# Kernel tuning notes

Hardware: AMD Instinct MI355X
Metric: run time of the kernel (lower is better)

The kernel has to match this reference:

```python
import jax, jax.numpy as jnp
import numpy as np

N_NODES = 50000
N_EDGES = 600000
F_IN = 128
F_OUT = 128


def setup_inputs() -> dict:
    key = jax.random.key(0)
    k1, k2, k3, k4 = jax.random.split(key, 4)
    x = jax.random.normal(k1, (N_NODES, F_IN), dtype=jnp.float32)
    edge_index = jax.random.randint(k2, (2, N_EDGES), 0, N_NODES, dtype=jnp.int64)
    # Linear weights stored as [in, out] so out = h @ W + b
    scale = 1.0 / np.sqrt(F_IN)
    W_l = jax.random.uniform(k3, (F_IN, F_OUT), jnp.float32, -scale, scale)
    W_r = jax.random.uniform(k4, (F_IN, F_OUT), jnp.float32, -scale, scale)
    b_l = jnp.zeros((F_OUT,), jnp.float32)
    b_r = jnp.zeros((F_OUT,), jnp.float32)
    return {"x": x, "edge_index": edge_index, "W_l": W_l, "b_l": b_l, "W_r": W_r, "b_r": b_r}


def reference(x, edge_index, W_l, b_l, W_r, b_r):
    num_nodes = x.shape[0]
    src, dst = edge_index[0], edge_index[1]
    # P2_Gather: source node features per edge  [E, F]
    x_j = x[src]
    # P3_ScatterAdd: sum over incoming edges per destination node  [N, F]
    sum_agg = jax.ops.segment_sum(x_j, dst, num_segments=num_nodes)
    # P3_ScatterAdd_Count: in-degree per node  [N]
    count = jax.ops.segment_sum(jnp.ones_like(dst, dtype=x.dtype), dst,
                                num_segments=num_nodes)
    # P4_ElewiseDiv: mean aggregation (avoid div-by-zero for isolated nodes)
    mean_agg = sum_agg / jnp.maximum(count, 1.0)[:, None]
    # P1_Matmul_Dual + P5_ElewiseAct
    out = mean_agg @ W_l + b_l + x @ W_r + b_r
    return jax.nn.relu(out)
```

## Files before the change

kernel.cpp:

```cpp
#include <hip/hip_runtime.h>

#define NN 50000
#define NE 600000
#define FD 128
#define MAXS 62

using short8  = __attribute__((ext_vector_type(8))) short;
using ushort8 = __attribute__((ext_vector_type(8))) unsigned short;
using f32x4   = __attribute__((ext_vector_type(4))) float;
using f32x2   = __attribute__((ext_vector_type(2))) float;

__device__ __forceinline__ unsigned short f2bf(float f) {
    unsigned int u = __float_as_uint(f);
    return (unsigned short)((u + 0x7FFFu + ((u >> 16) & 1u)) >> 16);
}
__device__ __forceinline__ float bf2f(unsigned short u) {
    return __uint_as_float(((unsigned int)u) << 16);
}

#if __has_builtin(__builtin_amdgcn_cvt_pk_f32_fp8) && __has_builtin(__builtin_amdgcn_cvt_pk_fp8_f32)
#define FP8_HW 1
#else
#define FP8_HW 0
#endif

__device__ __forceinline__ unsigned int sw_enc(float f) {
    unsigned u = __float_as_uint(f);
    unsigned s = (u >> 24) & 0x80u;
    unsigned a = u & 0x7FFFFFFFu;
    if (a < 0x3C800000u) return s;
    unsigned r = a + 0x7FFFFu + ((a >> 20) & 1u);
    unsigned e = r >> 23;
    unsigned m = (r >> 20) & 7u;
    return s | ((e - 120u) << 3) | m;
}
__device__ __forceinline__ float sw_dec(unsigned b) {
    unsigned em = b & 0x7Fu;
    unsigned u  = ((b & 0x80u) << 24) | ((em + 960u) << 20);
    return em ? __uint_as_float(u) : 0.0f;
}

__device__ __forceinline__ unsigned int enc4(float a, float b, float c, float d) {
#if FP8_HW
    unsigned int w = 0;
    w = __builtin_amdgcn_cvt_pk_fp8_f32(a, b, w, false);
    w = __builtin_amdgcn_cvt_pk_fp8_f32(c, d, w, true);
    return w;
#else
    return sw_enc(a) | (sw_enc(b) << 8) | (sw_enc(c) << 16) | (sw_enc(d) << 24);
#endif
}

__device__ __forceinline__ void dec4_fma(unsigned int dw, float w, float* a) {
#if FP8_HW
    f32x2 lo = __builtin_amdgcn_cvt_pk_f32_fp8(dw, false);
    f32x2 hi = __builtin_amdgcn_cvt_pk_f32_fp8(dw, true);
    a[0] = fmaf(w, lo[0], a[0]); a[1] = fmaf(w, lo[1], a[1]);
    a[2] = fmaf(w, hi[0], a[2]); a[3] = fmaf(w, hi[1], a[3]);
#else
    a[0] = fmaf(w, sw_dec(dw & 0xFFu),         a[0]);
    a[1] = fmaf(w, sw_dec((dw >> 8) & 0xFFu),  a[1]);
    a[2] = fmaf(w, sw_dec((dw >> 16) & 0xFFu), a[2]);
    a[3] = fmaf(w, sw_dec(dw >> 24),           a[3]);
#endif
}

#define OFF_SLOT  200192
#define OFF_XQ    6600192
#define OFF_XB    13000192
#define OFF_MEANB 25800192
#define OFF_WBT   38600192
#define WS_NEED   (38600192 + 65536)

#define NXB 3125
#define NWB 16
#define NZC 196

__global__ __launch_bounds__(256) void prep_k(const float* __restrict__ x,
                                              const float* __restrict__ Wl,
                                              const float* __restrict__ Wr,
                                              unsigned short* __restrict__ xb,
                                              unsigned int* __restrict__ xq,
                                              unsigned short* __restrict__ wbT,
                                              unsigned int* __restrict__ slotw) {
    int b = blockIdx.x;
    if (b < NXB) {
        int i = b * 256 + threadIdx.x;
        const float4* p = reinterpret_cast<const float4*>(x) + (size_t)i * 2;
        float4 a = p[0], c = p[1];
        short8 r;
        r[0] = (short)f2bf(a.x); r[1] = (short)f2bf(a.y);
        r[2] = (short)f2bf(a.z); r[3] = (short)f2bf(a.w);
        r[4] = (short)f2bf(c.x); r[5] = (short)f2bf(c.y);
        r[6] = (short)f2bf(c.z); r[7] = (short)f2bf(c.w);
        reinterpret_cast<short8*>(xb)[i] = r;
        uint2 q;
        q.x = enc4(a.x, a.y, a.z, a.w);
        q.y = enc4(c.x, c.y, c.z, c.w);
        reinterpret_cast<uint2*>(xq)[i] = q;
    } else if (b < NXB + NWB) {
        int u = (b - NXB) * 256 + threadIdx.x;
        int col = u & 127;
        int kb  = (u >> 7) * 8;
        short8 r;
        #pragma unroll
        for (int j = 0; j < 8; ++j) {
            int k = kb + j;
            float w = (k < 128) ? Wl[(size_t)k * FD + col]
                                : Wr[(size_t)(k - 128) * FD + col];
            r[j] = (short)f2bf(w);
        }
        *reinterpret_cast<short8*>(&wbT[col * 256 + kb]) = r;
    } else {
        int i = (b - NXB - NWB) * 256 + threadIdx.x;
        if (i < NN) slotw[(size_t)i * 32] = 0;
    }
}

__global__ __launch_bounds__(256) void scatter_slot_k(const int* __restrict__ ei,
                                                      unsigned int* __restrict__ slotw) {
    int e = blockIdx.x * 256 + threadIdx.x;
    if (e >= NE) return;
    int s = ei[e];
    int d = ei[NE + e];
    unsigned int* row = slotw + (size_t)d * 32;
    int p = atomicAdd((int*)row, 1);
    if (p < MAXS) reinterpret_cast<unsigned short*>(row)[2 + p] = (unsigned short)s;
}

__global__ __launch_bounds__(256) void gather_k(
    const unsigned int* __restrict__ xq,
    const unsigned int* __restrict__ slotw,
    unsigned short* __restrict__ meanb)
{
    int t = blockIdx.x * 256 + threadIdx.x;
    int n = t >> 3;
    if (n >= NN) return;
    const int l = t & 7;

    const unsigned int* row = slotw + (size_t)n * 32;
    uint4 h = *reinterpret_cast<const uint4*>(row);
    int cnt = (int)h.x;
    int dc  = cnt < MAXS ? cnt : MAXS;

    float a[16];
    #pragma unroll
    for (int k = 0; k < 16; ++k) a[k] = 0.f;

    {
        unsigned sA[6] = {h.y & 0xFFFFu, h.y >> 16, h.z & 0xFFFFu,
                          h.z >> 16, h.w & 0xFFFFu, h.w >> 16};
        #pragma unroll
        for (int j = 0; j < 6; ++j) {
            bool m  = j < dc;
            int  sj = m ? (int)sA[j] : 0;
            float w = m ? 1.0f : 0.0f;
            uint4 v = *reinterpret_cast<const uint4*>(
                xq + (size_t)sj * (FD / 4) + l * 4);
            dec4_fma(v.x, w, a);
            dec4_fma(v.y, w, a + 4);
            dec4_fma(v.z, w, a + 8);
            dec4_fma(v.w, w, a + 12);
        }
    }
    const unsigned short* rus = reinterpret_cast<const unsigned short*>(row);
    for (int base = 6; base < dc; base += 8) {
        ushort8 q = *reinterpret_cast<const ushort8*>(rus + 2 + base);
        #pragma unroll
        for (int j = 0; j < 8; ++j) {
            bool m  = (base + j) < dc;
            int  sj = m ? (int)q[j] : 0;
            float w = m ? 1.0f : 0.0f;
            uint4 v = *reinterpret_cast<const uint4*>(
                xq + (size_t)sj * (FD / 4) + l * 4);
            dec4_fma(v.x, w, a);
            dec4_fma(v.y, w, a + 4);
            dec4_fma(v.z, w, a + 8);
            dec4_fma(v.w, w, a + 12);
        }
    }
    float inv = 1.0f / fmaxf((float)cnt, 1.0f);
    short8 r0, r1;
    #pragma unroll
    for (int j = 0; j < 8; ++j) r0[j] = (short)f2bf(a[j] * inv);
    #pragma unroll
    for (int j = 0; j < 8; ++j) r1[j] = (short)f2bf(a[8 + j] * inv);
    unsigned short* mp = meanb + (size_t)n * FD + l * 16;
    *reinterpret_cast<short8*>(mp)     = r0;
    *reinterpret_cast<short8*>(mp + 8) = r1;
}

__global__ __launch_bounds__(512) void gemm_k(
    const unsigned short* __restrict__ xb,
    const unsigned short* __restrict__ meanb,
    const unsigned short* __restrict__ wbT,
    const float* __restrict__ bl, const float* __restrict__ br,
    float* __restrict__ out)
{
    __shared__ __align__(16) unsigned short Bt[128][72];

    const int tid   = threadIdx.x;
    const int lane  = tid & 63;
    const int wid   = tid >> 6;
    const int node0 = blockIdx.x * 64;

    const int rowq   = wid & 3;
    const int colh   = wid >> 2;
    const int arow_l = rowq * 16 + (lane & 15);
    const int arow   = node0 + arow_l;
    const int kgrp   = (lane >> 4) * 8;
    const int scol   = tid & 127;
    const int kb0    = (tid >> 7) * 16;

    f32x4 acc[4];
    #pragma unroll
    for (int c = 0; c < 4; ++c) acc[c] = (f32x4){0.f, 0.f, 0.f, 0.f};

    #pragma unroll
    for (int kc = 0; kc < 4; ++kc) {
        if (kc) __syncthreads();
        *reinterpret_cast<short8*>(&Bt[scol][kb0]) =
            *reinterpret_cast<const short8*>(&wbT[scol * 256 + kc * 64 + kb0]);
        *reinterpret_cast<short8*>(&Bt[scol][kb0 + 8]) =
            *reinterpret_cast<const short8*>(&wbT[scol * 256 + kc * 64 + kb0 + 8]);
        __syncthreads();

        #pragma unroll
        for (int ks = 0; ks < 2; ++ks) {
            int k0l = ks * 32 + kgrp;
            int k0g = kc * 64 + k0l;
            short8 af = {0, 0, 0, 0, 0, 0, 0, 0};
            if (arow < NN) {
                const unsigned short* base = (kc < 2) ? meanb : xb;
                int off = (kc < 2) ? k0g : (k0g - 128);
                af = *reinterpret_cast<const short8*>(base + (size_t)arow * FD + off);
            }
            #pragma unroll
            for (int c = 0; c < 4; ++c) {
                short8 bf = *reinterpret_cast<const short8*>(
                    &Bt[colh * 64 + c * 16 + (lane & 15)][k0l]);
                acc[c] = __builtin_amdgcn_mfma_f32_16x16x32_bf16(af, bf, acc[c], 0, 0, 0);
            }
        }
    }

    const int rbase = node0 + rowq * 16 + ((lane >> 4) << 2);
    #pragma unroll
    for (int c = 0; c < 4; ++c) {
        int col = colh * 64 + c * 16 + (lane & 15);
        float bsum_ = bl[col] + br[col];
        #pragma unroll
        for (int r = 0; r < 4; ++r) {
            int gr = rbase + r;
            if (gr < NN) {
                float v = acc[c][r] + bsum_;
                out[(size_t)gr * FD + col] = v > 0.f ? v : 0.f;
            }
        }
    }
}

#define FOFF_ROWPTR 0
#define FOFF_CURSOR 200064
#define FOFF_CSR    400128
#define FOFF_BSUM   2800384

__global__ __launch_bounds__(256) void hist_k(const int* __restrict__ ei,
                                              int* __restrict__ deg) {
    int e = blockIdx.x * 256 + threadIdx.x;
    if (e < NE) atomicAdd(&deg[ei[NE + e]], 1);
}

__global__ __launch_bounds__(256) void scan1_k(const int* __restrict__ deg,
                                               int* __restrict__ row_ptr,
                                               int* __restrict__ bsum) {
    __shared__ int ws[4];
    int i = blockIdx.x * 256 + threadIdx.x;
    int v = (i < NN) ? deg[i] : 0;
    int lane = threadIdx.x & 63, wid = threadIdx.x >> 6;
    int val = v;
    #pragma unroll
    for (int off = 1; off < 64; off <<= 1) {
        int t = __shfl_up(val, off);
        if (lane >= off) val += t;
    }
    if (lane == 63) ws[wid] = val;
    __syncthreads();
    int pre = 0;
    #pragma unroll
    for (int w = 0; w < 4; ++w) if (w < wid) pre += ws[w];
    val += pre;
    if (i < NN) row_ptr[i + 1] = val;
    if (threadIdx.x == 255) bsum[blockIdx.x] = val;
}

__global__ __launch_bounds__(256) void scan23_k(int* __restrict__ row_ptr,
                                                int* __restrict__ cursor,
                                                const int* __restrict__ bsum) {
    __shared__ int wsum[4];
    int t = threadIdx.x;
    int v = (t < (int)blockIdx.x) ? bsum[t] : 0;
    int lane = t & 63, wid = t >> 6;
    int val = v;
    #pragma unroll
    for (int off = 32; off; off >>= 1) val += __shfl_xor(val, off);
    if (lane == 0) wsum[wid] = val;
    __syncthreads();
    int offset = wsum[0] + wsum[1] + wsum[2] + wsum[3];
    int i = blockIdx.x * 256 + t;
    if (i == 0) row_ptr[0] = 0;
    if (i < NN) {
        int incl = row_ptr[i + 1] + offset;
        int d = cursor[i];
        row_ptr[i + 1] = incl;
        cursor[i] = incl - d;
    }
}

__global__ __launch_bounds__(256) void fill_k(const int* __restrict__ ei,
                                              int* __restrict__ cursor,
                                              int* __restrict__ csr_src) {
    int e = blockIdx.x * 256 + threadIdx.x;
    if (e < NE) {
        int s = ei[e];
        int d = ei[NE + e];
        int p = atomicAdd(&cursor[d], 1);
        csr_src[p] = s;
    }
}

__global__ __launch_bounds__(256) void agg_f32_k(const float* __restrict__ x,
                                                 const int* __restrict__ row_ptr,
                                                 const int* __restrict__ csr_src,
                                                 float* __restrict__ out) {
    int t = blockIdx.x * 256 + threadIdx.x;
    int n = t >> 5;
    if (n >= NN) return;
    int l = t & 31;
    int beg = row_ptr[n], end = row_ptr[n + 1];
    float4 a0 = make_float4(0.f, 0.f, 0.f, 0.f);
    float4 a1 = make_float4(0.f, 0.f, 0.f, 0.f);
    const float4* x4 = reinterpret_cast<const float4*>(x);
    int e = beg;
    for (; e + 1 < end; e += 2) {
        int s0 = csr_src[e], s1 = csr_src[e + 1];
        float4 v0 = x4[(size_t)s0 * 32 + l];
        float4 v1 = x4[(size_t)s1 * 32 + l];
        a0.x += v0.x; a0.y += v0.y; a0.z += v0.z; a0.w += v0.w;
        a1.x += v1.x; a1.y += v1.y; a1.z += v1.z; a1.w += v1.w;
    }
    if (e < end) {
        int s0 = csr_src[e];
        float4 v0 = x4[(size_t)s0 * 32 + l];
        a0.x += v0.x; a0.y += v0.y; a0.z += v0.z; a0.w += v0.w;
    }
    float inv = 1.0f / fmaxf((float)(end - beg), 1.0f);
    float4 r;
    r.x = (a0.x + a1.x) * inv; r.y = (a0.y + a1.y) * inv;
    r.z = (a0.z + a1.z) * inv; r.w = (a0.w + a1.w) * inv;
    reinterpret_cast<float4*>(out)[(size_t)n * 32 + l] = r;
}

__global__ __launch_bounds__(256) void gemm_f32_k(
    float* __restrict__ out, const float* __restrict__ x,
    const float* __restrict__ Wl, const float* __restrict__ bl,
    const float* __restrict__ Wr, const float* __restrict__ br)
{
    __shared__ __align__(16) unsigned short Btf[128][136];
    const int tid  = threadIdx.x;
    const int lane = tid & 63;
    const int wid  = tid >> 6;
    const int row0 = blockIdx.x * 64 + wid * 16;
    const int arow = row0 + (lane & 15);
    const bool rok = arow < NN;
    const int kgrp = (lane >> 4) * 8;
    f32x4 acc[8];
    #pragma unroll
    for (int c = 0; c < 8; ++c) acc[c] = (f32x4){0.f, 0.f, 0.f, 0.f};
    const int scol  = tid & 127;
    const int shalf = tid >> 7;
    #pragma unroll
    for (int p = 0; p < 2; ++p) {
        if (p) __syncthreads();
        const float* W = p ? Wr : Wl;
        #pragma unroll
        for (int kk = 0; kk < 64; kk += 8) {
            int kb = shalf * 64 + kk;
            short8 w;
            #pragma unroll
            for (int j = 0; j < 8; ++j) w[j] = (short)f2bf(W[(size_t)(kb + j) * FD + scol]);
            *reinterpret_cast<short8*>(&Btf[scol][kb]) = w;
        }
        __syncthreads();
        #pragma unroll
        for (int ks = 0; ks < 4; ++ks) {
            int k0 = ks * 32 + kgrp;
            short8 af = {0, 0, 0, 0, 0, 0, 0, 0};
            if (rok) {
                const float* ap = (p ? x : out) + (size_t)arow * FD + k0;
                float4 v0 = *reinterpret_cast<const float4*>(ap);
                float4 v1 = *reinterpret_cast<const float4*>(ap + 4);
                af[0] = (short)f2bf(v0.x); af[1] = (short)f2bf(v0.y);
                af[2] = (short)f2bf(v0.z); af[3] = (short)f2bf(v0.w);
                af[4] = (short)f2bf(v1.x); af[5] = (short)f2bf(v1.y);
                af[6] = (short)f2bf(v1.z); af[7] = (short)f2bf(v1.w);
            }
            #pragma unroll
            for (int c = 0; c < 8; ++c) {
                short8 bf = *reinterpret_cast<const short8*>(&Btf[c * 16 + (lane & 15)][k0]);
                acc[c] = __builtin_amdgcn_mfma_f32_16x16x32_bf16(af, bf, acc[c], 0, 0, 0);
            }
        }
    }
    const int rbase = row0 + ((lane >> 4) << 2);
    #pragma unroll
    for (int c = 0; c < 8; ++c) {
        int col = c * 16 + (lane & 15);
        float bsum_ = bl[col] + br[col];
        #pragma unroll
        for (int r = 0; r < 4; ++r) {
            int gr = rbase + r;
            if (gr < NN) {
                float v = acc[c][r] + bsum_;
                out[(size_t)gr * FD + col] = v > 0.f ? v : 0.f;
            }
        }
    }
}

extern "C" void kernel_launch(void* const* d_in, const int* in_sizes, int n_in,
                              void* d_out, int out_size, void* d_ws, size_t ws_size,
                              hipStream_t stream) {
    const float* x  = (const float*)d_in[0];
    const int*   ei = (const int*)d_in[1];
    const float* Wl = (const float*)d_in[2];
    const float* bl = (const float*)d_in[3];
    const float* Wr = (const float*)d_in[4];
    const float* br = (const float*)d_in[5];
    float* out = (float*)d_out;
    char* ws = (char*)d_ws;

    if (ws_size >= WS_NEED) {
        unsigned int*   slotw = (unsigned int*)(ws + OFF_SLOT);
        unsigned int*   xq    = (unsigned int*)(ws + OFF_XQ);
        unsigned short* xb    = (unsigned short*)(ws + OFF_XB);
        unsigned short* meanb = (unsigned short*)(ws + OFF_MEANB);
        unsigned short* wbT   = (unsigned short*)(ws + OFF_WBT);

        prep_k        <<<NXB + NWB + NZC, 256, 0, stream>>>(x, Wl, Wr, xb, xq, wbT, slotw);
        scatter_slot_k<<<(NE + 255) / 256, 256, 0, stream>>>(ei, slotw);
        gather_k      <<<(NN * 8 + 255) / 256, 256, 0, stream>>>(xq, slotw, meanb);
        gemm_k        <<<(NN + 63) / 64, 512, 0, stream>>>(xb, meanb, wbT, bl, br, out);
    } else {
        int* row_ptr = (int*)(ws + FOFF_ROWPTR);
        int* cursor  = (int*)(ws + FOFF_CURSOR);
        int* csr_src = (int*)(ws + FOFF_CSR);
        int* bsum    = (int*)(ws + FOFF_BSUM);

        hipMemsetAsync(cursor, 0, (size_t)NN * sizeof(int), stream);
        hist_k  <<<(NE + 255) / 256, 256, 0, stream>>>(ei, cursor);
        scan1_k <<<196, 256, 0, stream>>>(cursor, row_ptr, bsum);
        scan23_k<<<196, 256, 0, stream>>>(row_ptr, cursor, bsum);
        fill_k  <<<(NE + 255) / 256, 256, 0, stream>>>(ei, cursor, csr_src);
        agg_f32_k<<<(NN * 32 + 255) / 256, 256, 0, stream>>>(x, row_ptr, csr_src, out);
        gemm_f32_k<<<(NN + 63) / 64, 256, 0, stream>>>(out, x, Wl, bl, Wr, br);
    }
}
```

Before: 80.75 us.

## Fuse mean aggregation into GEMM kernel via shared-memory staging

The separate gather kernel is merged into the GEMM kernel. Each 512-thread block first aggregates the FP8 neighbor features for its 64 nodes, writes the bf16 means into LDS, syncs, and then feeds them straight into the MFMA loop. This removes the global round trip of the bf16 mean buffer and one kernel launch. In exchange, LDS use per block rises by about 17KB, and the irregular gather can no longer overlap with the GEMM phase inside a block.

```diff
diff --git a/kernel.cpp b/kernel.cpp
--- a/kernel.cpp
+++ b/kernel.cpp
@@ -13,9 +13,6 @@
 __device__ __forceinline__ unsigned short f2bf(float f) {
     unsigned int u = __float_as_uint(f);
     return (unsigned short)((u + 0x7FFFu + ((u >> 16) & 1u)) >> 16);
-}
-__device__ __forceinline__ float bf2f(unsigned short u) {
-    return __uint_as_float(((unsigned int)u) << 16);
 }
 
 #if __has_builtin(__builtin_amdgcn_cvt_pk_f32_fp8) && __has_builtin(__builtin_amdgcn_cvt_pk_fp8_f32)
@@ -68,9 +65,8 @@
 #define OFF_SLOT  200192
 #define OFF_XQ    6600192
 #define OFF_XB    13000192
-#define OFF_MEANB 25800192
-#define OFF_WBT   38600192
-#define WS_NEED   (38600192 + 65536)
+#define OFF_WBT   25800192
+#define WS_NEED   (25800192 + 65536)
 
 #define NXB 3125
 #define NWB 16
@@ -128,81 +124,79 @@
     if (p < MAXS) reinterpret_cast<unsigned short*>(row)[2 + p] = (unsigned short)s;
 }
 
-__global__ __launch_bounds__(256) void gather_k(
+__global__ __launch_bounds__(512) void agg_gemm_k(
     const unsigned int* __restrict__ xq,
     const unsigned int* __restrict__ slotw,
-    unsigned short* __restrict__ meanb)
-{
-    int t = blockIdx.x * 256 + threadIdx.x;
-    int n = t >> 3;
-    if (n >= NN) return;
-    const int l = t & 7;
-
-    const unsigned int* row = slotw + (size_t)n * 32;
-    uint4 h = *reinterpret_cast<const uint4*>(row);
-    int cnt = (int)h.x;
-    int dc  = cnt < MAXS ? cnt : MAXS;
-
-    float a[16];
-    #pragma unroll
-    for (int k = 0; k < 16; ++k) a[k] = 0.f;
-
-    {
-        unsigned sA[6] = {h.y & 0xFFFFu, h.y >> 16, h.z & 0xFFFFu,
-                          h.z >> 16, h.w & 0xFFFFu, h.w >> 16};
-        #pragma unroll
-        for (int j = 0; j < 6; ++j) {
-            bool m  = j < dc;
-            int  sj = m ? (int)sA[j] : 0;
-            float w = m ? 1.0f : 0.0f;
-            uint4 v = *reinterpret_cast<const uint4*>(
-                xq + (size_t)sj * (FD / 4) + l * 4);
-            dec4_fma(v.x, w, a);
-            dec4_fma(v.y, w, a + 4);
-            dec4_fma(v.z, w, a + 8);
-            dec4_fma(v.w, w, a + 12);
-        }
-    }
-    const unsigned short* rus = reinterpret_cast<const unsigned short*>(row);
-    for (int base = 6; base < dc; base += 8) {
-        ushort8 q = *reinterpret_cast<const ushort8*>(rus + 2 + base);
-        #pragma unroll
-        for (int j = 0; j < 8; ++j) {
-            bool m  = (base + j) < dc;
-            int  sj = m ? (int)q[j] : 0;
-            float w = m ? 1.0f : 0.0f;
-            uint4 v = *reinterpret_cast<const uint4*>(
-                xq + (size_t)sj * (FD / 4) + l * 4);
-            dec4_fma(v.x, w, a);
-            dec4_fma(v.y, w, a + 4);
-            dec4_fma(v.z, w, a + 8);
-            dec4_fma(v.w, w, a + 12);
-        }
-    }
-    float inv = 1.0f / fmaxf((float)cnt, 1.0f);
-    short8 r0, r1;
-    #pragma unroll
-    for (int j = 0; j < 8; ++j) r0[j] = (short)f2bf(a[j] * inv);
-    #pragma unroll
-    for (int j = 0; j < 8; ++j) r1[j] = (short)f2bf(a[8 + j] * inv);
-    unsigned short* mp = meanb + (size_t)n * FD + l * 16;
-    *reinterpret_cast<short8*>(mp)     = r0;
-    *reinterpret_cast<short8*>(mp + 8) = r1;
-}
-
-__global__ __launch_bounds__(512) void gemm_k(
     const unsigned short* __restrict__ xb,
-    const unsigned short* __restrict__ meanb,
     const unsigned short* __restrict__ wbT,
     const float* __restrict__ bl, const float* __restrict__ br,
     float* __restrict__ out)
 {
+    __shared__ __align__(16) unsigned short meanS[64][136];
     __shared__ __align__(16) unsigned short Bt[128][72];
 
     const int tid   = threadIdx.x;
     const int lane  = tid & 63;
     const int wid   = tid >> 6;
     const int node0 = blockIdx.x * 64;
+
+    {
+        const int nl = tid >> 3;
+        const int l  = tid & 7;
+        const int n  = node0 + nl;
+
+        float a[16];
+        #pragma unroll
+        for (int k = 0; k < 16; ++k) a[k] = 0.f;
+        float inv = 0.f;
+
+        if (n < NN) {
+            const unsigned int* row = slotw + (size_t)n * 32;
+            uint4 h = *reinterpret_cast<const uint4*>(row);
+            int cnt = (int)h.x;
+            int dc  = cnt < MAXS ? cnt : MAXS;
+
+            unsigned sA[6] = {h.y & 0xFFFFu, h.y >> 16, h.z & 0xFFFFu,
+                              h.z >> 16, h.w & 0xFFFFu, h.w >> 16};
+            #pragma unroll
+            for (int j = 0; j < 6; ++j) {
+                bool m  = j < dc;
+                int  sj = m ? (int)sA[j] : 0;
+                float w = m ? 1.0f : 0.0f;
+                uint4 v = *reinterpret_cast<const uint4*>(
+                    xq + (size_t)sj * (FD / 4) + l * 4);
+                dec4_fma(v.x, w, a);
+                dec4_fma(v.y, w, a + 4);
+                dec4_fma(v.z, w, a + 8);
+                dec4_fma(v.w, w, a + 12);
+            }
+            const unsigned short* rus = reinterpret_cast<const unsigned short*>(row);
+            for (int base = 6; base < dc; base += 8) {
+                ushort8 q = *reinterpret_cast<const ushort8*>(rus + 2 + base);
+                #pragma unroll
+                for (int j = 0; j < 8; ++j) {
+                    bool m  = (base + j) < dc;
+                    int  sj = m ? (int)q[j] : 0;
+                    float w = m ? 1.0f : 0.0f;
+                    uint4 v = *reinterpret_cast<const uint4*>(
+                        xq + (size_t)sj * (FD / 4) + l * 4);
+                    dec4_fma(v.x, w, a);
+                    dec4_fma(v.y, w, a + 4);
+                    dec4_fma(v.z, w, a + 8);
+                    dec4_fma(v.w, w, a + 12);
+                }
+            }
+            inv = 1.0f / fmaxf((float)cnt, 1.0f);
+        }
+        short8 r0, r1;
+        #pragma unroll
+        for (int j = 0; j < 8; ++j) r0[j] = (short)f2bf(a[j] * inv);
+        #pragma unroll
+        for (int j = 0; j < 8; ++j) r1[j] = (short)f2bf(a[8 + j] * inv);
+        *reinterpret_cast<short8*>(&meanS[nl][l * 16])     = r0;
+        *reinterpret_cast<short8*>(&meanS[nl][l * 16 + 8]) = r1;
+    }
+    __syncthreads();
 
     const int rowq   = wid & 3;
     const int colh   = wid >> 2;
@@ -230,10 +224,11 @@
             int k0l = ks * 32 + kgrp;
             int k0g = kc * 64 + k0l;
             short8 af = {0, 0, 0, 0, 0, 0, 0, 0};
-            if (arow < NN) {
-                const unsigned short* base = (kc < 2) ? meanb : xb;
-                int off = (kc < 2) ? k0g : (k0g - 128);
-                af = *reinterpret_cast<const short8*>(base + (size_t)arow * FD + off);
+            if (kc < 2) {
+                af = *reinterpret_cast<const short8*>(&meanS[arow_l][k0g]);
+            } else if (arow < NN) {
+                af = *reinterpret_cast<const short8*>(
+                    xb + (size_t)arow * FD + (k0g - 128));
             }
             #pragma unroll
             for (int c = 0; c < 4; ++c) {
@@ -444,13 +439,12 @@
         unsigned int*   slotw = (unsigned int*)(ws + OFF_SLOT);
         unsigned int*   xq    = (unsigned int*)(ws + OFF_XQ);
         unsigned short* xb    = (unsigned short*)(ws + OFF_XB);
-        unsigned short* meanb = (unsigned short*)(ws + OFF_MEANB);
         unsigned short* wbT   = (unsigned short*)(ws + OFF_WBT);
 
         prep_k        <<<NXB + NWB + NZC, 256, 0, stream>>>(x, Wl, Wr, xb, xq, wbT, slotw);
         scatter_slot_k<<<(NE + 255) / 256, 256, 0, stream>>>(ei, slotw);
-        gather_k      <<<(NN * 8 + 255) / 256, 256, 0, stream>>>(xq, slotw, meanb);
-        gemm_k        <<<(NN + 63) / 64, 512, 0, stream>>>(xb, meanb, wbT, bl, br, out);
+        agg_gemm_k    <<<(NN + 63) / 64, 512, 0, stream>>>(xq, slotw, xb, wbT,
+                                                           bl, br, out);
     } else {
         int* row_ptr = (int*)(ws + FOFF_ROWPTR);
         int* cursor  = (int*)(ws + FOFF_CURSOR);
```

Result: faster. 77.50 us (-4.0%).
